# Kernel tuning notes

Measured on AMD Instinct MI355X. Metric: run time of the kernel, lower is better.

## Reference

```python
import jax, jax.numpy as jnp
import numpy as np

ALPHA = 0.2      # GAT leaky_relu slope (args.alpha)
MLP_SLOPE = 0.01 # F.leaky_relu default in the MLP path
NEG = -9e15

def _l2_normalize(x, axis=1, eps=1e-12):
    n = jnp.sqrt(jnp.sum(x * x, axis=axis, keepdims=True))
    return x / jnp.maximum(n, eps)

def setup_inputs() -> dict:
    key = jax.random.key(0)
    ks = jax.random.split(key, 14)
    N, Din, Dh, H, Dg, M1, M2, E = 8192, 512, 256, 2, 512, 512, 256, 100000
    x = jax.random.normal(ks[0], (N, Din), dtype=jnp.float32)
    adj = jax.random.randint(ks[1], (N, N), 0, 2, dtype=jnp.int32)
    train_sample = jax.random.randint(ks[2], (E, 2), 0, N, dtype=jnp.int32)
    llm_emb = jax.random.normal(ks[3], (N, Dg), dtype=jnp.float32)
    # GAT head params (stacked over heads)
    Wg = jax.random.normal(ks[4], (H, Din, Dh), dtype=jnp.float32) * 0.05
    a1 = jax.random.normal(ks[5], (H, Dh), dtype=jnp.float32) * 0.05
    a2 = jax.random.normal(ks[6], (H, Dh), dtype=jnp.float32) * 0.05
    bias_g = jnp.zeros((H, Dh), dtype=jnp.float32)
    # MLP params
    W1 = jax.random.normal(ks[7], (Dh + Dg, M1), dtype=jnp.float32) * 0.03
    b1 = jnp.zeros((M1,), dtype=jnp.float32)
    W2 = jax.random.normal(ks[8], (M1, M2), dtype=jnp.float32) * 0.04
    b2 = jnp.zeros((M2,), dtype=jnp.float32)
    return {"x": x, "adj": adj, "train_sample": train_sample, "llm_emb": llm_emb,
            "Wg": Wg, "a1": a1, "a2": a2, "bias_g": bias_g,
            "W1": W1, "b1": b1, "W2": W2, "b2": b2}

def reference(x, adj, train_sample, llm_emb, Wg, a1, a2, bias_g, W1, b1, W2, b2):
    mask = adj > 0  # [N, N]

    def head(W, av1, av2, b):
        h = x @ W                                   # [N, Dh]
        s1 = h @ av1                                # [N]
        s2 = h @ av2                                # [N]
        e = jax.nn.leaky_relu(s1[:, None] + s2[None, :], ALPHA)  # [N, N]
        att = jax.nn.softmax(jnp.where(mask, e, NEG), axis=1)
        out = att @ h                               # [N, Dh]
        out = jax.nn.leaky_relu(out, ALPHA)
        out = _l2_normalize(out, axis=1)
        return out + b

    # encode: single GNN layer -> mean over heads (dropout inactive in eval)
    out_heads = jax.vmap(head)(Wg, a1, a2, bias_g)  # [H, N, Dh]
    embed_gnn = jnp.mean(out_heads, axis=0)         # [N, Dh]
    embed = jnp.concatenate([llm_emb, embed_gnn], axis=1)  # [N, Dg+Dh]

    def mlp(z):
        z = jax.nn.leaky_relu(z @ W1 + b1, MLP_SLOPE)
        z = jax.nn.leaky_relu(z @ W2 + b2, MLP_SLOPE)
        return z

    tf_embed = mlp(embed)
    target_embed = mlp(embed)
    train_tf = tf_embed[train_sample[:, 0]]
    train_tg = target_embed[train_sample[:, 1]]
    pred = jnp.sum(train_tf * train_tg, axis=1, keepdims=True)  # dot decode, [E,1]
    return pred
```

## Files before the change

kernel.cpp:

```cpp
#include <hip/hip_runtime.h>
#include <hip/hip_bf16.h>
#include <cstdint>
#include <cstddef>

#define ALPHA 0.2f
#define MLP_SLOPE 0.01f

typedef short bf16x8 __attribute__((ext_vector_type(8)));
typedef float f32x4 __attribute__((ext_vector_type(4)));
typedef unsigned short ushort_t;

#define ASM_BARRIER() __asm__ __volatile__("s_waitcnt lgkmcnt(0)\n\ts_barrier" ::: "memory")

__device__ __forceinline__ float lrelu(float x, float s) { return x > 0.f ? x : x * s; }
__device__ __forceinline__ ushort_t f2bf(float x) {
  __hip_bfloat16 h = __float2bfloat16(x);
  return *reinterpret_cast<ushort_t*>(&h);
}
__device__ __forceinline__ float bf2f(ushort_t u) {
  union { unsigned int i; float f; } v; v.i = ((unsigned int)u) << 16; return v.f;
}

__global__ __launch_bounds__(256) void split_f(
    const float* __restrict__ in, ushort_t* __restrict__ hi,
    ushort_t* __restrict__ lo)
{
  int idx = blockIdx.x * 256 + threadIdx.x;
  float4 v = ((const float4*)in)[idx];
  ushort4 h, l;
  h.x = f2bf(v.x); l.x = f2bf(v.x - bf2f(h.x));
  h.y = f2bf(v.y); l.y = f2bf(v.y - bf2f(h.y));
  h.z = f2bf(v.z); l.z = f2bf(v.z - bf2f(h.z));
  h.w = f2bf(v.w); l.w = f2bf(v.w - bf2f(h.w));
  ((ushort4*)hi)[idx] = h;
  ((ushort4*)lo)[idx] = l;
}

__global__ __launch_bounds__(256) void pack_wt(
    const float* __restrict__ W, ushort_t* __restrict__ hi,
    ushort_t* __restrict__ lo, int K, int N)
{
  int gid = blockIdx.x * 256 + threadIdx.x;
  int lane = gid & 63;
  int kbc = K >> 5;
  int kblk = (gid >> 6) % kbc;
  int nblk = (gid >> 6) / kbc;
  size_t b = (size_t)blockIdx.y * K * N;
  int col = nblk * 16 + (lane & 15);
  int krow = kblk * 32 + (lane >> 4) * 8;
  ushort_t h[8] __attribute__((aligned(16)));
  ushort_t l[8] __attribute__((aligned(16)));
#pragma unroll
  for (int e = 0; e < 8; ++e) {
    float v = W[b + (size_t)(krow + e) * N + col];
    h[e] = f2bf(v);
    l[e] = f2bf(v - bf2f(h[e]));
  }
  *(uint4*)&hi[b + (size_t)gid * 8] = *(uint4*)h;
  *(uint4*)&lo[b + (size_t)gid * 8] = *(uint4*)l;
}

__global__ __launch_bounds__(256) void gemm_nolds(
    const ushort_t* __restrict__ Ahi, const ushort_t* __restrict__ Alo,
    const ushort_t* __restrict__ Bph, const ushort_t* __restrict__ Bpl,
    const float* __restrict__ bias, float* __restrict__ Cf,
    ushort_t* __restrict__ Chi, ushort_t* __restrict__ Clo,
    int M, int N, int K, float slope, int act)
{
  const size_t boff = (size_t)blockIdx.z * N * K;
  const size_t coff = (size_t)blockIdx.z * M * N;
  const int t = threadIdx.x;
  const int wave = t >> 6, l63 = t & 63;
  const int l16 = t & 15, oct = (t >> 4) & 3, quad = oct;
  const int wm = (wave & 1) * 64, wn = (wave >> 1) * 32;
  const int m0 = blockIdx.y * 128 + wm;
  const int nb = blockIdx.x * 4 + (wave >> 1) * 2;
  const int nbase = blockIdx.x * 64 + wn;
  const int ksteps = K >> 5;

  const ushort_t* aph[4];
  const ushort_t* apl[4];
#pragma unroll
  for (int mt = 0; mt < 4; ++mt) {
    size_t o = (size_t)(m0 + mt * 16 + l16) * K + oct * 8;
    aph[mt] = Ahi + o;
    apl[mt] = Alo + o;
  }
  const ushort_t* bph[2];
  const ushort_t* bpl[2];
#pragma unroll
  for (int nt = 0; nt < 2; ++nt) {
    size_t o = boff + ((size_t)(nb + nt) * ksteps * 64 + l63) * 8;
    bph[nt] = Bph + o;
    bpl[nt] = Bpl + o;
  }

  f32x4 acc[4][2];
#pragma unroll
  for (int i = 0; i < 4; ++i)
#pragma unroll
    for (int j = 0; j < 2; ++j) acc[i][j] = (f32x4){0.f, 0.f, 0.f, 0.f};

#define LOADF(AH, AL, BH, BL, KB)                                         \
  {                                                                       \
    _Pragma("unroll") for (int mt = 0; mt < 4; ++mt) {                    \
      AH[mt] = *(const bf16x8*)(aph[mt] + (size_t)(KB) * 32);             \
      AL[mt] = *(const bf16x8*)(apl[mt] + (size_t)(KB) * 32);             \
    }                                                                     \
    _Pragma("unroll") for (int nt = 0; nt < 2; ++nt) {                    \
      BH[nt] = *(const bf16x8*)(bph[nt] + (size_t)(KB) * 512);            \
      BL[nt] = *(const bf16x8*)(bpl[nt] + (size_t)(KB) * 512);            \
    }                                                                     \
  }
#define MF(AH, AL, BH, BL)                                                \
  {                                                                       \
    _Pragma("unroll") for (int mt = 0; mt < 4; ++mt)                      \
    _Pragma("unroll") for (int nt = 0; nt < 2; ++nt) {                    \
      acc[mt][nt] = __builtin_amdgcn_mfma_f32_16x16x32_bf16(AH[mt], BH[nt], acc[mt][nt], 0, 0, 0); \
      acc[mt][nt] = __builtin_amdgcn_mfma_f32_16x16x32_bf16(AH[mt], BL[nt], acc[mt][nt], 0, 0, 0); \
      acc[mt][nt] = __builtin_amdgcn_mfma_f32_16x16x32_bf16(AL[mt], BH[nt], acc[mt][nt], 0, 0, 0); \
    }                                                                     \
  }

  bf16x8 ah0[4], al0[4], bh0[2], bl0[2];
  bf16x8 ah1[4], al1[4], bh1[2], bl1[2];
  LOADF(ah0, al0, bh0, bl0, 0)
  for (int kb = 0; kb < ksteps; kb += 2) {
    LOADF(ah1, al1, bh1, bl1, kb + 1)
    MF(ah0, al0, bh0, bl0)
    if (kb + 2 < ksteps) LOADF(ah0, al0, bh0, bl0, kb + 2)
    MF(ah1, al1, bh1, bl1)
  }
#undef LOADF
#undef MF

#pragma unroll
  for (int mt = 0; mt < 4; ++mt)
#pragma unroll
    for (int nt = 0; nt < 2; ++nt)
#pragma unroll
      for (int rg = 0; rg < 4; ++rg) {
        int m = m0 + mt * 16 + quad * 4 + rg;
        int n = nbase + nt * 16 + l16;
        float v = acc[mt][nt][rg];
        if (bias) v += bias[n];
        if (act) v = lrelu(v, slope);
        size_t o = coff + (size_t)m * N + n;
        if (Cf) Cf[o] = v;
        if (Chi) {
          ushort_t h = f2bf(v);
          Chi[o] = h; Clo[o] = f2bf(v - bf2f(h));
        }
      }
}

__global__ __launch_bounds__(256) void s_kernel(
    const float* __restrict__ hbuf, const float* __restrict__ a1,
    const float* __restrict__ a2, float* __restrict__ s1, float* __restrict__ s2)
{
  const int gw = (blockIdx.x * 256 + threadIdx.x) >> 6;
  const int lane = threadIdx.x & 63;
#pragma unroll
  for (int hh = 0; hh < 2; ++hh) {
    float4 hv = ((const float4*)(hbuf + ((size_t)hh * 8192 + gw) * 256))[lane];
    float4 a1v = ((const float4*)(a1 + hh * 256))[lane];
    float4 a2v = ((const float4*)(a2 + hh * 256))[lane];
    float p1 = hv.x * a1v.x + hv.y * a1v.y + hv.z * a1v.z + hv.w * a1v.w;
    float p2 = hv.x * a2v.x + hv.y * a2v.y + hv.z * a2v.z + hv.w * a2v.w;
    for (int off = 32; off > 0; off >>= 1) {
      p1 += __shfl_xor(p1, off);
      p2 += __shfl_xor(p2, off);
    }
    if (lane == 0) {
      s1[hh * 8192 + gw] = p1;
      s2[hh * 8192 + gw] = p2;
    }
  }
}

__global__ __launch_bounds__(256) void h_pack(
    const float* __restrict__ hbuf, ushort_t* __restrict__ Bpack)
{
  int gid = blockIdx.x * 256 + threadIdx.x;
  int lane = gid & 63;
  int ntile = (gid >> 6) & 15;
  int kblk = (gid >> 10) & 255;
  int head = gid >> 18;
  int c = ntile * 16 + (lane & 15);
  int jb = kblk * 32 + (lane >> 4) * 8;
  ushort_t o[8] __attribute__((aligned(16)));
#pragma unroll
  for (int e = 0; e < 8; ++e)
    o[e] = f2bf(hbuf[((size_t)head * 8192 + jb + e) * 256 + c]);
  *(uint4*)&Bpack[(size_t)gid * 8] = *(uint4*)o;
}

__global__ __launch_bounds__(256, 2) void attn_mfma4(
    const ushort_t* __restrict__ Bpack, const float* __restrict__ s1g,
    const float* __restrict__ s2g, const int* __restrict__ adj,
    ushort_t* __restrict__ pacc, float* __restrict__ pl)
{
  __shared__ ushort_t Wlds[2][2][4][64][8];
  const int t = threadIdx.x;
  const int i0 = blockIdx.x * 64;
  const int js = blockIdx.y;
  const int kbase = js * 2048;
  const int wr = t >> 2, kq = t & 3;
  const int glane = kq * 16 + (wr & 15);
  const int gmt = wr >> 4;
  const float s1v0 = s1g[i0 + wr];
  const float s1v1 = s1g[8192 + i0 + wr];
  const int wave = t >> 6, head = wave >> 1, nh = wave & 1;
  const int l16 = t & 15, quad = (t >> 4) & 3;
  const int l63 = t & 63;
  f32x4 acc[4][8];
#pragma unroll
  for (int m = 0; m < 4; ++m)
#pragma unroll
    for (int n = 0; n < 8; ++n) acc[m][n] = (f32x4){0.f, 0.f, 0.f, 0.f};
  float rs0 = 0.f, rs1 = 0.f;

  const int* arow = adj + (size_t)(i0 + wr) * 8192;
  int4 pa0, pa1;
  float4 p20a, p20b, p21a, p21b;
  {
    const int kk = kbase + kq * 8;
    pa0 = *(const int4*)&arow[kk];
    pa1 = *(const int4*)&arow[kk + 4];
    p20a = *(const float4*)&s2g[kk];
    p20b = *(const float4*)&s2g[kk + 4];
    p21a = *(const float4*)&s2g[8192 + kk];
    p21b = *(const float4*)&s2g[8192 + kk + 4];
  }
  for (int kt = 0; kt < 64; ++kt) {
    const int buf = kt & 1;
    const int kblk = js * 64 + kt;
    const ushort_t* bb =
        Bpack + ((((size_t)head * 256 + kblk) * 16 + nh * 8) * 64 + l63) * 8;
    bf16x8 Bf[8];
#pragma unroll
    for (int nt = 0; nt < 8; ++nt)
      Bf[nt] = *(const bf16x8*)&bb[nt * 512];

    {
      int am[8] = {pa0.x, pa0.y, pa0.z, pa0.w, pa1.x, pa1.y, pa1.z, pa1.w};
      float s20[8] = {p20a.x, p20a.y, p20a.z, p20a.w, p20b.x, p20b.y, p20b.z, p20b.w};
      float s21[8] = {p21a.x, p21a.y, p21a.z, p21a.w, p21b.x, p21b.y, p21b.z, p21b.w};
      ushort_t w0[8] __attribute__((aligned(16)));
      ushort_t w1[8] __attribute__((aligned(16)));
#pragma unroll
      for (int e = 0; e < 8; ++e) {
        float e0 = s1v0 + s20[e];
        float e1 = s1v1 + s21[e];
        e0 = fmaxf(e0, 0.f) + ALPHA * fminf(e0, 0.f);
        e1 = fmaxf(e1, 0.f) + ALPHA * fminf(e1, 0.f);
        float v0 = am[e] > 0 ? __expf(e0) : 0.f;
        float v1 = am[e] > 0 ? __expf(e1) : 0.f;
        rs0 += v0; rs1 += v1;
        w0[e] = f2bf(v0); w1[e] = f2bf(v1);
      }
      *(uint4*)&Wlds[buf][0][gmt][glane][0] = *(uint4*)w0;
      *(uint4*)&Wlds[buf][1][gmt][glane][0] = *(uint4*)w1;
    }
    if (kt < 63) {
      const int kk = kbase + (kt + 1) * 32 + kq * 8;
      pa0 = *(const int4*)&arow[kk];
      pa1 = *(const int4*)&arow[kk + 4];
      p20a = *(const float4*)&s2g[kk];
      p20b = *(const float4*)&s2g[kk + 4];
      p21a = *(const float4*)&s2g[8192 + kk];
      p21b = *(const float4*)&s2g[8192 + kk + 4];
    }
    ASM_BARRIER();
    bf16x8 Af[4];
#pragma unroll
    for (int mt = 0; mt < 4; ++mt)
      Af[mt] = *(const bf16x8*)&Wlds[buf][head][mt][l63][0];
#pragma unroll
    for (int mt = 0; mt < 4; ++mt)
#pragma unroll
      for (int nt = 0; nt < 8; ++nt)
        acc[mt][nt] = __builtin_amdgcn_mfma_f32_16x16x32_bf16(
            Af[mt], Bf[nt], acc[mt][nt], 0, 0, 0);
  }
  rs0 += __shfl_xor(rs0, 1); rs0 += __shfl_xor(rs0, 2);
  rs1 += __shfl_xor(rs1, 1); rs1 += __shfl_xor(rs1, 2);
  if (kq == 0) {
    pl[((size_t)js * 2 + 0) * 8192 + i0 + wr] = rs0;
    pl[((size_t)js * 2 + 1) * 8192 + i0 + wr] = rs1;
  }
  const int n0 = nh * 128;
#pragma unroll
  for (int mt = 0; mt < 4; ++mt)
#pragma unroll
    for (int nt = 0; nt < 8; ++nt)
#pragma unroll
      for (int rg = 0; rg < 4; ++rg) {
        int row = i0 + mt * 16 + quad * 4 + rg;
        int col = n0 + nt * 16 + l16;
        pacc[(((size_t)js * 2 + head) * 8192 + row) * 256 + col] =
            f2bf(acc[mt][nt][rg]);
      }
}

__global__ __launch_bounds__(256) void attn_finalize(
    const ushort_t* __restrict__ pacc, const float* __restrict__ pl,
    const float* __restrict__ bg, const float* __restrict__ llm,
    float* __restrict__ embed)
{
  __shared__ float red[256];
  const int r = blockIdx.x;
  const int t = threadIdx.x;
  if (t < 128)
    *(float4*)&embed[(size_t)r * 768 + t * 4] =
        *(const float4*)&llm[(size_t)r * 512 + t * 4];
  float o[2], nrm[2];
#pragma unroll
  for (int hh = 0; hh < 2; ++hh) {
    float num = 0.f, l = 0.f;
#pragma unroll
    for (int js = 0; js < 4; ++js) {
      num += bf2f(pacc[(((size_t)js * 2 + hh) * 8192 + r) * 256 + t]);
      l += pl[((size_t)js * 2 + hh) * 8192 + r];
    }
    o[hh] = lrelu(num / l, ALPHA);
  }
  for (int hh = 0; hh < 2; ++hh) {
    __syncthreads();
    red[t] = o[hh] * o[hh];
    __syncthreads();
    for (int s = 128; s > 0; s >>= 1) {
      if (t < s) red[t] += red[t + s];
      __syncthreads();
    }
    nrm[hh] = fmaxf(sqrtf(red[0]), 1e-12f);
  }
  embed[(size_t)r * 768 + 512 + t] =
      0.5f * (o[0] / nrm[0] + bg[t] + o[1] / nrm[1] + bg[256 + t]);
}

__global__ __launch_bounds__(256) void pred_kernel(
    const float* __restrict__ z2, const int* __restrict__ ts,
    float* __restrict__ out, int E)
{
  const int gw = (blockIdx.x * 256 + threadIdx.x) >> 6;
  const int lane = threadIdx.x & 63;
  if (gw >= E) return;
  const int a = ts[gw * 2], b = ts[gw * 2 + 1];
  float4 va = ((const float4*)(z2 + (size_t)a * 256))[lane];
  float4 vb = ((const float4*)(z2 + (size_t)b * 256))[lane];
  float p = va.x * vb.x + va.y * vb.y + va.z * vb.z + va.w * vb.w;
  for (int off = 32; off > 0; off >>= 1) p += __shfl_xor(p, off);
  if (lane == 0) out[gw] = p;
}

extern "C" void kernel_launch(void* const* d_in, const int* in_sizes, int n_in,
                              void* d_out, int out_size, void* d_ws, size_t ws_size,
                              hipStream_t stream) {
  const float* x   = (const float*)d_in[0];
  const int*   adj = (const int*)d_in[1];
  const int*   ts  = (const int*)d_in[2];
  const float* llm = (const float*)d_in[3];
  const float* Wg  = (const float*)d_in[4];
  const float* a1  = (const float*)d_in[5];
  const float* a2  = (const float*)d_in[6];
  const float* bg  = (const float*)d_in[7];
  const float* W1  = (const float*)d_in[8];
  const float* b1  = (const float*)d_in[9];
  const float* W2  = (const float*)d_in[10];
  const float* b2  = (const float*)d_in[11];
  float* out = (float*)d_out;
  float* ws  = (float*)d_ws;
  const int E = in_sizes[2] / 2;

  float*    hbuf  = ws;
  ushort_t* Bpack = (ushort_t*)(ws + 4194304);
  float*    embed = ws;
  ushort_t* xhi   = (ushort_t*)(ws + 6291456);
  ushort_t* xlo   = (ushort_t*)(ws + 8388608);
  ushort_t* z1hi  = xhi;
  ushort_t* z1lo  = xlo;
  float*    s1    = ws + 10485760;
  float*    s2    = ws + 10502144;
  float*    pl    = ws + 10518528;
  ushort_t* pacc  = (ushort_t*)(ws + 10584064);
  ushort_t* ehi   = (ushort_t*)(ws + 10584064);
  ushort_t* elo   = (ushort_t*)(ws + 13729792);
  float*    z2    = ws + 16875520;
  ushort_t* wgphi = (ushort_t*)(ws + 18972672);
  ushort_t* wgplo = (ushort_t*)(ws + 19103744);
  ushort_t* w1phi = (ushort_t*)(ws + 19234816);
  ushort_t* w1plo = (ushort_t*)(ws + 19431424);
  ushort_t* w2phi = (ushort_t*)(ws + 19628032);
  ushort_t* w2plo = (ushort_t*)(ws + 19693568);

  split_f<<<4096, 256, 0, stream>>>(x, xhi, xlo);
  pack_wt<<<dim3(64, 2), 256, 0, stream>>>(Wg, wgphi, wgplo, 512, 256);
  pack_wt<<<dim3(192, 1), 256, 0, stream>>>(W1, w1phi, w1plo, 768, 512);
  pack_wt<<<dim3(64, 1), 256, 0, stream>>>(W2, w2phi, w2plo, 512, 256);
  gemm_nolds<<<dim3(4, 64, 2), 256, 0, stream>>>(
      xhi, xlo, wgphi, wgplo, nullptr, hbuf, nullptr, nullptr,
      8192, 256, 512, 0.f, 0);
  s_kernel<<<2048, 256, 0, stream>>>(hbuf, a1, a2, s1, s2);
  h_pack<<<2048, 256, 0, stream>>>(hbuf, Bpack);
  attn_mfma4<<<dim3(128, 4), 256, 0, stream>>>(Bpack, s1, s2, adj, pacc, pl);
  attn_finalize<<<8192, 256, 0, stream>>>(pacc, pl, bg, llm, embed);
  split_f<<<6144, 256, 0, stream>>>(embed, ehi, elo);
  gemm_nolds<<<dim3(8, 64, 1), 256, 0, stream>>>(
      ehi, elo, w1phi, w1plo, b1, nullptr, z1hi, z1lo,
      8192, 512, 768, MLP_SLOPE, 1);
  gemm_nolds<<<dim3(4, 64, 1), 256, 0, stream>>>(
      z1hi, z1lo, w2phi, w2plo, b2, z2, nullptr, nullptr,
      8192, 256, 512, MLP_SLOPE, 1);
  pred_kernel<<<(E * 64 + 255) / 256, 256, 0, stream>>>(z2, ts, out, E);
}
```

Baseline: 663.3 us.

## Remove LDS staging in attention kernel; each wave computes its own weight fragments

The attention kernel's work split changes so that each wave owns 16 rows and all 256 output columns for both heads. Each lane builds the bf16 attention-weight A fragment directly in registers, which removes the LDS round trip and the per-iteration barrier. B fragments are streamed in groups through a three-slot register ring, so global loads overlap the MFMAs. The cost is that every wave now loads the full B tile for both heads, quadrupling per-wave B traffic with no sharing across waves. The 32 accumulator tiles also raise register pressure, which may affect occupancy.

```diff
diff --git a/kernel.cpp b/kernel.cpp
--- a/kernel.cpp
+++ b/kernel.cpp
@@ -9,8 +9,6 @@
 typedef short bf16x8 __attribute__((ext_vector_type(8)));
 typedef float f32x4 __attribute__((ext_vector_type(4)));
 typedef unsigned short ushort_t;
-
-#define ASM_BARRIER() __asm__ __volatile__("s_waitcnt lgkmcnt(0)\n\ts_barrier" ::: "memory")
 
 __device__ __forceinline__ float lrelu(float x, float s) { return x > 0.f ? x : x * s; }
 __device__ __forceinline__ ushort_t f2bf(float x) {
@@ -195,36 +193,35 @@
   *(uint4*)&Bpack[(size_t)gid * 8] = *(uint4*)o;
 }
 
-__global__ __launch_bounds__(256, 2) void attn_mfma4(
+__global__ __launch_bounds__(256, 2) void attn_mfma5(
     const ushort_t* __restrict__ Bpack, const float* __restrict__ s1g,
     const float* __restrict__ s2g, const int* __restrict__ adj,
     ushort_t* __restrict__ pacc, float* __restrict__ pl)
 {
-  __shared__ ushort_t Wlds[2][2][4][64][8];
   const int t = threadIdx.x;
   const int i0 = blockIdx.x * 64;
   const int js = blockIdx.y;
   const int kbase = js * 2048;
-  const int wr = t >> 2, kq = t & 3;
-  const int glane = kq * 16 + (wr & 15);
-  const int gmt = wr >> 4;
-  const float s1v0 = s1g[i0 + wr];
-  const float s1v1 = s1g[8192 + i0 + wr];
-  const int wave = t >> 6, head = wave >> 1, nh = wave & 1;
-  const int l16 = t & 15, quad = (t >> 4) & 3;
+  const int wq = t >> 6;
   const int l63 = t & 63;
-  f32x4 acc[4][8];
-#pragma unroll
-  for (int m = 0; m < 4; ++m)
-#pragma unroll
-    for (int n = 0; n < 8; ++n) acc[m][n] = (f32x4){0.f, 0.f, 0.f, 0.f};
+  const int l16 = t & 15, oct = (t >> 4) & 3;
+  const int row = i0 + wq * 16 + l16;
+
+  const float s1v0 = s1g[row];
+  const float s1v1 = s1g[8192 + row];
+  const int* arow = adj + (size_t)row * 8192;
+
+  f32x4 acc[2][16];
+#pragma unroll
+  for (int h = 0; h < 2; ++h)
+#pragma unroll
+    for (int n = 0; n < 16; ++n) acc[h][n] = (f32x4){0.f, 0.f, 0.f, 0.f};
   float rs0 = 0.f, rs1 = 0.f;
 
-  const int* arow = adj + (size_t)(i0 + wr) * 8192;
   int4 pa0, pa1;
   float4 p20a, p20b, p21a, p21b;
   {
-    const int kk = kbase + kq * 8;
+    const int kk = kbase + oct * 8;
     pa0 = *(const int4*)&arow[kk];
     pa1 = *(const int4*)&arow[kk + 4];
     p20a = *(const float4*)&s2g[kk];
@@ -232,16 +229,22 @@
     p21a = *(const float4*)&s2g[8192 + kk];
     p21b = *(const float4*)&s2g[8192 + kk + 4];
   }
+
   for (int kt = 0; kt < 64; ++kt) {
-    const int buf = kt & 1;
     const int kblk = js * 64 + kt;
-    const ushort_t* bb =
-        Bpack + ((((size_t)head * 256 + kblk) * 16 + nh * 8) * 64 + l63) * 8;
-    bf16x8 Bf[8];
-#pragma unroll
-    for (int nt = 0; nt < 8; ++nt)
-      Bf[nt] = *(const bf16x8*)&bb[nt * 512];
-
+    const ushort_t* bb0 = Bpack + ((size_t)kblk * 16 * 64 + l63) * 8;
+    const ushort_t* bb1 = bb0 + (size_t)256 * 16 * 64 * 8;
+
+    bf16x8 Bf[3][4];
+    auto loadg = [&](int g, int slot) {
+      const ushort_t* p = (g < 4 ? bb0 : bb1) + (size_t)((g & 3) * 4) * 512;
+#pragma unroll
+      for (int i = 0; i < 4; ++i) Bf[slot][i] = *(const bf16x8*)(p + i * 512);
+    };
+    loadg(0, 0);
+    loadg(1, 1);
+
+    bf16x8 Af0, Af1;
     {
       int am[8] = {pa0.x, pa0.y, pa0.z, pa0.w, pa1.x, pa1.y, pa1.z, pa1.w};
       float s20[8] = {p20a.x, p20a.y, p20a.z, p20a.w, p20b.x, p20b.y, p20b.z, p20b.w};
@@ -259,11 +262,12 @@
         rs0 += v0; rs1 += v1;
         w0[e] = f2bf(v0); w1[e] = f2bf(v1);
       }
-      *(uint4*)&Wlds[buf][0][gmt][glane][0] = *(uint4*)w0;
-      *(uint4*)&Wlds[buf][1][gmt][glane][0] = *(uint4*)w1;
-    }
+      Af0 = *(const bf16x8*)w0;
+      Af1 = *(const bf16x8*)w1;
+    }
+
     if (kt < 63) {
-      const int kk = kbase + (kt + 1) * 32 + kq * 8;
+      const int kk = kbase + (kt + 1) * 32 + oct * 8;
       pa0 = *(const int4*)&arow[kk];
       pa1 = *(const int4*)&arow[kk + 4];
       p20a = *(const float4*)&s2g[kk];
@@ -271,35 +275,36 @@
       p21a = *(const float4*)&s2g[8192 + kk];
       p21b = *(const float4*)&s2g[8192 + kk + 4];
     }
-    ASM_BARRIER();
-    bf16x8 Af[4];
-#pragma unroll
-    for (int mt = 0; mt < 4; ++mt)
-      Af[mt] = *(const bf16x8*)&Wlds[buf][head][mt][l63][0];
-#pragma unroll
-    for (int mt = 0; mt < 4; ++mt)
-#pragma unroll
-      for (int nt = 0; nt < 8; ++nt)
-        acc[mt][nt] = __builtin_amdgcn_mfma_f32_16x16x32_bf16(
-            Af[mt], Bf[nt], acc[mt][nt], 0, 0, 0);
-  }
-  rs0 += __shfl_xor(rs0, 1); rs0 += __shfl_xor(rs0, 2);
-  rs1 += __shfl_xor(rs1, 1); rs1 += __shfl_xor(rs1, 2);
-  if (kq == 0) {
-    pl[((size_t)js * 2 + 0) * 8192 + i0 + wr] = rs0;
-    pl[((size_t)js * 2 + 1) * 8192 + i0 + wr] = rs1;
-  }
-  const int n0 = nh * 128;
-#pragma unroll
-  for (int mt = 0; mt < 4; ++mt)
-#pragma unroll
-    for (int nt = 0; nt < 8; ++nt)
+
+#pragma unroll
+    for (int g = 0; g < 8; ++g) {
+      if (g + 2 < 8) loadg(g + 2, (g + 2) % 3);
+      const bf16x8 Af = (g < 4) ? Af0 : Af1;
+      const int h = g >> 2, nb = (g & 3) * 4;
+#pragma unroll
+      for (int i = 0; i < 4; ++i)
+        acc[h][nb + i] = __builtin_amdgcn_mfma_f32_16x16x32_bf16(
+            Af, Bf[g % 3][i], acc[h][nb + i], 0, 0, 0);
+    }
+  }
+
+  rs0 += __shfl_xor(rs0, 16); rs0 += __shfl_xor(rs0, 32);
+  rs1 += __shfl_xor(rs1, 16); rs1 += __shfl_xor(rs1, 32);
+  if (oct == 0) {
+    pl[((size_t)js * 2 + 0) * 8192 + row] = rs0;
+    pl[((size_t)js * 2 + 1) * 8192 + row] = rs1;
+  }
+
+#pragma unroll
+  for (int h = 0; h < 2; ++h)
+#pragma unroll
+    for (int nt = 0; nt < 16; ++nt)
 #pragma unroll
       for (int rg = 0; rg < 4; ++rg) {
-        int row = i0 + mt * 16 + quad * 4 + rg;
-        int col = n0 + nt * 16 + l16;
-        pacc[(((size_t)js * 2 + head) * 8192 + row) * 256 + col] =
-            f2bf(acc[mt][nt][rg]);
+        int r = i0 + wq * 16 + oct * 4 + rg;
+        int c = nt * 16 + l16;
+        pacc[(((size_t)js * 2 + h) * 8192 + r) * 256 + c] =
+            f2bf(acc[h][nt][rg]);
       }
 }
 
@@ -403,7 +408,7 @@
       8192, 256, 512, 0.f, 0);
   s_kernel<<<2048, 256, 0, stream>>>(hbuf, a1, a2, s1, s2);
   h_pack<<<2048, 256, 0, stream>>>(hbuf, Bpack);
-  attn_mfma4<<<dim3(128, 4), 256, 0, stream>>>(Bpack, s1, s2, adj, pacc, pl);
+  attn_mfma5<<<dim3(128, 4), 256, 0, stream>>>(Bpack, s1, s2, adj, pacc, pl);
   attn_finalize<<<8192, 256, 0, stream>>>(pacc, pl, bg, llm, embed);
   split_f<<<6144, 256, 0, stream>>>(embed, ehi, elo);
   gemm_nolds<<<dim3(8, 64, 1), 256, 0, stream>>>(
```

After: 797.5 us. +20.2%, slower.

## Software-pipeline attention weight generation behind MFMA and use shuffle reduction in finalize

Applied to the files above, without the earlier changes.

The attention kernel now produces the softmax weight tile for the next k-block after issuing the MFMAs for the current block. The first tile is generated before the loop and adjacency/s2 loads run two iterations ahead, so the exp/bf16 conversion VALU work and the LDS writes can overlap matrix-core execution. This leaves a single barrier per iteration. Separately, the finalize kernel replaces its tree reduction over shared memory, which needed many __syncthreads, with wave shuffles plus one barrier. Holding the extra prefetched values raises register pressure in a kernel already constrained by launch_bounds(256,2).

```diff
diff --git a/kernel.cpp b/kernel.cpp
--- a/kernel.cpp
+++ b/kernel.cpp
@@ -195,7 +195,7 @@
   *(uint4*)&Bpack[(size_t)gid * 8] = *(uint4*)o;
 }
 
-__global__ __launch_bounds__(256, 2) void attn_mfma4(
+__global__ __launch_bounds__(256, 2) void attn_mfma6(
     const ushort_t* __restrict__ Bpack, const float* __restrict__ s1g,
     const float* __restrict__ s2g, const int* __restrict__ adj,
     ushort_t* __restrict__ pacc, float* __restrict__ pl)
@@ -223,17 +223,43 @@
   const int* arow = adj + (size_t)(i0 + wr) * 8192;
   int4 pa0, pa1;
   float4 p20a, p20b, p21a, p21b;
-  {
-    const int kk = kbase + kq * 8;
+
+  auto fetch = [&](int kk) {
     pa0 = *(const int4*)&arow[kk];
     pa1 = *(const int4*)&arow[kk + 4];
     p20a = *(const float4*)&s2g[kk];
     p20b = *(const float4*)&s2g[kk + 4];
     p21a = *(const float4*)&s2g[8192 + kk];
     p21b = *(const float4*)&s2g[8192 + kk + 4];
-  }
+  };
+  auto gen = [&](int buf) {
+    int am[8] = {pa0.x, pa0.y, pa0.z, pa0.w, pa1.x, pa1.y, pa1.z, pa1.w};
+    float s20[8] = {p20a.x, p20a.y, p20a.z, p20a.w, p20b.x, p20b.y, p20b.z, p20b.w};
+    float s21[8] = {p21a.x, p21a.y, p21a.z, p21a.w, p21b.x, p21b.y, p21b.z, p21b.w};
+    ushort_t w0[8] __attribute__((aligned(16)));
+    ushort_t w1[8] __attribute__((aligned(16)));
+#pragma unroll
+    for (int e = 0; e < 8; ++e) {
+      float e0 = s1v0 + s20[e];
+      float e1 = s1v1 + s21[e];
+      e0 = fmaxf(e0, 0.f) + ALPHA * fminf(e0, 0.f);
+      e1 = fmaxf(e1, 0.f) + ALPHA * fminf(e1, 0.f);
+      float v0 = am[e] > 0 ? __expf(e0) : 0.f;
+      float v1 = am[e] > 0 ? __expf(e1) : 0.f;
+      rs0 += v0; rs1 += v1;
+      w0[e] = f2bf(v0); w1[e] = f2bf(v1);
+    }
+    *(uint4*)&Wlds[buf][0][gmt][glane][0] = *(uint4*)w0;
+    *(uint4*)&Wlds[buf][1][gmt][glane][0] = *(uint4*)w1;
+  };
+
+  fetch(kbase + kq * 8);
+  gen(0);
+  fetch(kbase + 32 + kq * 8);
+  ASM_BARRIER();
+
   for (int kt = 0; kt < 64; ++kt) {
-    const int buf = kt & 1;
+    const int cur = kt & 1, nxt = cur ^ 1;
     const int kblk = js * 64 + kt;
     const ushort_t* bb =
         Bpack + ((((size_t)head * 256 + kblk) * 16 + nh * 8) * 64 + l63) * 8;
@@ -241,48 +267,23 @@
 #pragma unroll
     for (int nt = 0; nt < 8; ++nt)
       Bf[nt] = *(const bf16x8*)&bb[nt * 512];
-
-    {
-      int am[8] = {pa0.x, pa0.y, pa0.z, pa0.w, pa1.x, pa1.y, pa1.z, pa1.w};
-      float s20[8] = {p20a.x, p20a.y, p20a.z, p20a.w, p20b.x, p20b.y, p20b.z, p20b.w};
-      float s21[8] = {p21a.x, p21a.y, p21a.z, p21a.w, p21b.x, p21b.y, p21b.z, p21b.w};
-      ushort_t w0[8] __attribute__((aligned(16)));
-      ushort_t w1[8] __attribute__((aligned(16)));
-#pragma unroll
-      for (int e = 0; e < 8; ++e) {
-        float e0 = s1v0 + s20[e];
-        float e1 = s1v1 + s21[e];
-        e0 = fmaxf(e0, 0.f) + ALPHA * fminf(e0, 0.f);
-        e1 = fmaxf(e1, 0.f) + ALPHA * fminf(e1, 0.f);
-        float v0 = am[e] > 0 ? __expf(e0) : 0.f;
-        float v1 = am[e] > 0 ? __expf(e1) : 0.f;
-        rs0 += v0; rs1 += v1;
-        w0[e] = f2bf(v0); w1[e] = f2bf(v1);
-      }
-      *(uint4*)&Wlds[buf][0][gmt][glane][0] = *(uint4*)w0;
-      *(uint4*)&Wlds[buf][1][gmt][glane][0] = *(uint4*)w1;
-    }
-    if (kt < 63) {
-      const int kk = kbase + (kt + 1) * 32 + kq * 8;
-      pa0 = *(const int4*)&arow[kk];
-      pa1 = *(const int4*)&arow[kk + 4];
-      p20a = *(const float4*)&s2g[kk];
-      p20b = *(const float4*)&s2g[kk + 4];
-      p21a = *(const float4*)&s2g[8192 + kk];
-      p21b = *(const float4*)&s2g[8192 + kk + 4];
-    }
-    ASM_BARRIER();
     bf16x8 Af[4];
 #pragma unroll
     for (int mt = 0; mt < 4; ++mt)
-      Af[mt] = *(const bf16x8*)&Wlds[buf][head][mt][l63][0];
+      Af[mt] = *(const bf16x8*)&Wlds[cur][head][mt][l63][0];
 #pragma unroll
     for (int mt = 0; mt < 4; ++mt)
 #pragma unroll
       for (int nt = 0; nt < 8; ++nt)
         acc[mt][nt] = __builtin_amdgcn_mfma_f32_16x16x32_bf16(
             Af[mt], Bf[nt], acc[mt][nt], 0, 0, 0);
-  }
+    if (kt < 63) {
+      gen(nxt);
+      if (kt < 62) fetch(kbase + (kt + 2) * 32 + kq * 8);
+    }
+    ASM_BARRIER();
+  }
+
   rs0 += __shfl_xor(rs0, 1); rs0 += __shfl_xor(rs0, 2);
   rs1 += __shfl_xor(rs1, 1); rs1 += __shfl_xor(rs1, 2);
   if (kq == 0) {
@@ -308,13 +309,14 @@
     const float* __restrict__ bg, const float* __restrict__ llm,
     float* __restrict__ embed)
 {
-  __shared__ float red[256];
+  __shared__ float red[8];
   const int r = blockIdx.x;
   const int t = threadIdx.x;
+  const int wv = t >> 6, lane = t & 63;
   if (t < 128)
     *(float4*)&embed[(size_t)r * 768 + t * 4] =
         *(const float4*)&llm[(size_t)r * 512 + t * 4];
-  float o[2], nrm[2];
+  float o[2];
 #pragma unroll
   for (int hh = 0; hh < 2; ++hh) {
     float num = 0.f, l = 0.f;
@@ -325,18 +327,17 @@
     }
     o[hh] = lrelu(num / l, ALPHA);
   }
-  for (int hh = 0; hh < 2; ++hh) {
-    __syncthreads();
-    red[t] = o[hh] * o[hh];
-    __syncthreads();
-    for (int s = 128; s > 0; s >>= 1) {
-      if (t < s) red[t] += red[t + s];
-      __syncthreads();
-    }
-    nrm[hh] = fmaxf(sqrtf(red[0]), 1e-12f);
-  }
+  float v0 = o[0] * o[0], v1 = o[1] * o[1];
+  for (int off = 32; off > 0; off >>= 1) {
+    v0 += __shfl_xor(v0, off);
+    v1 += __shfl_xor(v1, off);
+  }
+  if (lane == 0) { red[wv] = v0; red[4 + wv] = v1; }
+  __syncthreads();
+  float n0 = fmaxf(sqrtf(red[0] + red[1] + red[2] + red[3]), 1e-12f);
+  float n1 = fmaxf(sqrtf(red[4] + red[5] + red[6] + red[7]), 1e-12f);
   embed[(size_t)r * 768 + 512 + t] =
-      0.5f * (o[0] / nrm[0] + bg[t] + o[1] / nrm[1] + bg[256 + t]);
+      0.5f * (o[0] / n0 + bg[t] + o[1] / n1 + bg[256 + t]);
 }
 
 __global__ __launch_bounds__(256) void pred_kernel(
@@ -403,7 +404,7 @@
       8192, 256, 512, 0.f, 0);
   s_kernel<<<2048, 256, 0, stream>>>(hbuf, a1, a2, s1, s2);
   h_pack<<<2048, 256, 0, stream>>>(hbuf, Bpack);
-  attn_mfma4<<<dim3(128, 4), 256, 0, stream>>>(Bpack, s1, s2, adj, pacc, pl);
+  attn_mfma6<<<dim3(128, 4), 256, 0, stream>>>(Bpack, s1, s2, adj, pacc, pl);
   attn_finalize<<<8192, 256, 0, stream>>>(pacc, pl, bg, llm, embed);
   split_f<<<6144, 256, 0, stream>>>(embed, ehi, elo);
   gemm_nolds<<<dim3(8, 64, 1), 256, 0, stream>>>(
```

Result: no change. 658.7 us (-0.7%).
